# Kernel optimization log

Measured on AMD Instinct MI355X. Metric: run time of the kernel, lower is better.

The kernel has to match this reference:

```python
import jax, jax.numpy as jnp
import numpy as np

B, T, D, F = 32, 512, 512, 256
K = 3
MEL_MAX = 4096
EPS = 1e-5


def _xavier(key, shape, fan_in, fan_out):
    lim = float(np.sqrt(6.0 / (fan_in + fan_out)))
    return jax.random.uniform(key, shape, jnp.float32, -lim, lim)


def setup_inputs() -> dict:
    key = jax.random.key(0)
    ks = jax.random.split(key, 6)
    x = jax.random.normal(ks[0], (B, T, D), jnp.float32)
    target = jax.random.randint(ks[1], (B, T), 0, 8)  # per-token durations
    # conv weights stored as [K, I, O] (lax 'WIO'); torch xavier on [O,I,K]: fan_in=I*K, fan_out=O*K
    w1 = _xavier(ks[2], (K, D, F), D * K, F * K)
    b1 = jnp.zeros((F,), jnp.float32)
    g1 = jnp.ones((F,), jnp.float32)
    be1 = jnp.zeros((F,), jnp.float32)
    w2 = _xavier(ks[3], (K, F, F), F * K, F * K)
    b2 = jnp.zeros((F,), jnp.float32)
    g2 = jnp.ones((F,), jnp.float32)
    be2 = jnp.zeros((F,), jnp.float32)
    wl = _xavier(ks[4], (F, 1), F, 1)
    bl = jnp.zeros((1,), jnp.float32)
    return dict(x=x, target=target, mel_max_length=MEL_MAX,
                w1=w1, b1=b1, g1=g1, be1=be1,
                w2=w2, b2=b2, g2=g2, be2=be2, wl=wl, bl=bl)


def _layer_norm(h, g, b):
    mu = jnp.mean(h, axis=-1, keepdims=True)
    var = jnp.mean(jnp.square(h - mu), axis=-1, keepdims=True)
    return (h - mu) * jax.lax.rsqrt(var + EPS) * g + b


def _conv1d(h, w, b):
    # h: [B,T,C_in], w: [K,C_in,C_out]; torch padding=1 with K=3 == SAME
    out = jax.lax.conv_general_dilated(h, w, (1,), 'SAME',
                                       dimension_numbers=('NWC', 'WIO', 'NWC'))
    return out + b


def reference(x, target, mel_max_length, w1, b1, g1, be1, w2, b2, g2, be2, wl, bl):
    # ---- DurationPredictor (eval: dropout = identity) ----
    h = jax.nn.relu(_layer_norm(_conv1d(x, w1, b1), g1, be1))
    h = jax.nn.relu(_layer_norm(_conv1d(h, w2, b2), g2, be2))
    dur_pred = jax.nn.relu(h @ wl + bl)[..., 0]  # [B, T]

    # ---- LR: ragged expansion of x by `target` durations, padded to mel_max_length ----
    cum = jnp.cumsum(target, axis=1)              # [B, T]
    total = cum[:, -1]                            # [B]
    pos = jnp.arange(mel_max_length)              # [M]
    # frame m maps to token i with cum[i-1] <= m < cum[i]
    idx = jax.vmap(lambda c: jnp.searchsorted(c, pos, side='right'))(cum)  # [B, M]
    idx = jnp.clip(idx, 0, x.shape[1] - 1)
    mask = pos[None, :] < total[:, None]          # [B, M]
    out = jnp.take_along_axis(x, idx[..., None], axis=1) * mask[..., None].astype(x.dtype)
    return (out, dur_pred)
```

## Files before the change

### kernel.cpp

```cpp
#include <hip/hip_runtime.h>
#include <type_traits>

#define B_   32
#define T_   512
#define D_   512
#define F_   256
#define MEL  4096
#define EPS_ 1e-5f

typedef __attribute__((ext_vector_type(8))) short bf16x8;
typedef __attribute__((ext_vector_type(4))) float f32x4;

#define GLL16(gp, lp) \
    __builtin_amdgcn_global_load_lds((const __attribute__((address_space(1))) void*)(gp), \
                                     (__attribute__((address_space(3))) void*)(lp), 16, 0, 0)
#define BARRIER() do { asm volatile("" ::: "memory"); __builtin_amdgcn_s_barrier(); \
                       asm volatile("" ::: "memory"); } while (0)
#define MEMPIN() asm volatile("" ::: "memory")

__device__ inline unsigned short f2bf(float f) {
    unsigned u = __float_as_uint(f);
    unsigned r = (u + 0x7fff + ((u >> 16) & 1)) >> 16;
    return (unsigned short)r;
}

#define PREP_WBLOCKS 2304

__global__ __launch_bounds__(256)
void prep_kernel(const float* __restrict__ w1, const float* __restrict__ w2,
                 const int* __restrict__ tgt,
                 unsigned short* __restrict__ w1T, unsigned short* __restrict__ w2T,
                 int* __restrict__ gidx)
{
    __shared__ int lcum[T_];
    __shared__ int wsum[4];

    int bid = blockIdx.x;
    int tid = threadIdx.x;
    if (bid < PREP_WBLOCKS) {
        int idx = bid * 256 + tid;
        if (idx < 3 * D_ * F_) {
            int kk = idx / F_, f = idx % F_;
            w1T[(size_t)f * (3 * D_) + kk] = f2bf(w1[idx]);
        } else {
            int j = idx - 3 * D_ * F_;
            int kk = j / F_, f = j % F_;
            w2T[(size_t)f * (3 * F_) + kk] = f2bf(w2[j]);
        }
        return;
    }

    int b = bid - PREP_WBLOCKS;
    int t0 = tid * 2;
    int a0 = tgt[b * T_ + t0], a1 = tgt[b * T_ + t0 + 1];
    int lane = tid & 63, w = tid >> 6;
    int v = a0 + a1;
#pragma unroll
    for (int o = 1; o < 64; o <<= 1) { int u = __shfl_up(v, o); if (lane >= o) v += u; }
    if (lane == 63) wsum[w] = v;
    __syncthreads();
    int base = 0;
#pragma unroll
    for (int i = 0; i < 4; ++i) if (i < w) base += wsum[i];
    int incl = base + v;
    lcum[t0]     = incl - a1;
    lcum[t0 + 1] = incl;
    __syncthreads();

    int total = lcum[T_ - 1];
#pragma unroll
    for (int k = 0; k < MEL / 256; ++k) {
        int pos = tid + k * 256;
        int lo = 0, hi = T_;
        while (lo < hi) { int mid = (lo + hi) >> 1; if (lcum[mid] <= pos) lo = mid + 1; else hi = mid; }
        gidx[b * MEL + pos] = (pos < total) ? min(lo, T_ - 1) : -1;
    }
}

template<int IN_D, typename InT, bool FUSE_DUR, int GPHASES, int GBASE>
__global__ __launch_bounds__(512)
void conv_mfma_kernel(const InT* __restrict__ x, const unsigned short* __restrict__ wT,
                      const float* __restrict__ bias, const float* __restrict__ gamma,
                      const float* __restrict__ beta, unsigned short* __restrict__ out,
                      const float* __restrict__ wl, const float* __restrict__ bl,
                      float* __restrict__ dur,
                      const float* __restrict__ xf, const int* __restrict__ gidx,
                      float* __restrict__ gout)
{
    constexpr int MT = 64;
    constexpr int KT = 3 * IN_D;
    constexpr int PHASES = KT / 64;

    __shared__ __align__(16) char xs_raw[(MT + 2) * IN_D * 2];
    __shared__ __align__(16) unsigned short xsB[2 * 16384];
    __shared__ float red[MT][8];
    __shared__ float redD[MT][4];

    const int blocksPerBatch = T_ / MT;
    const int b  = blockIdx.x / blocksPerBatch;
    const int t0 = (blockIdx.x % blocksPerBatch) * MT;
    const int l  = threadIdx.x & 63;
    const int wv = threadIdx.x >> 6;
    const int fg = wv & 3;
    const int rg = wv >> 2;

    constexpr int CH = (MT + 2) * IN_D / 8;
    for (int c = threadIdx.x; c < CH; c += 512) {
        int j  = c / (IN_D / 8);
        int d8 = (c % (IN_D / 8)) * 8;
        int t  = t0 - 1 + j;
        uint4 pk = make_uint4(0u, 0u, 0u, 0u);
        if (t >= 0 && t < T_) {
            if constexpr (std::is_same_v<InT, float>) {
                const float4* src = reinterpret_cast<const float4*>(&x[((size_t)b * T_ + t) * IN_D + d8]);
                float4 a0 = src[0], a1 = src[1];
                pk.x = (unsigned)f2bf(a0.x) | ((unsigned)f2bf(a0.y) << 16);
                pk.y = (unsigned)f2bf(a0.z) | ((unsigned)f2bf(a0.w) << 16);
                pk.z = (unsigned)f2bf(a1.x) | ((unsigned)f2bf(a1.y) << 16);
                pk.w = (unsigned)f2bf(a1.z) | ((unsigned)f2bf(a1.w) << 16);
            } else {
                pk = *reinterpret_cast<const uint4*>(&x[((size_t)b * T_ + t) * IN_D + d8]);
            }
        }
        int byte = ((j * IN_D + d8) * 2) ^ ((j & 7) << 4);
        *reinterpret_cast<uint4*>(&xs_raw[byte]) = pk;
    }

    float bv[4], gv[4], bev[4], wlv[4];
#pragma unroll
    for (int n = 0; n < 4; ++n) {
        int f = fg * 64 + n * 16 + (l & 15);
        bv[n] = bias[f]; gv[n] = gamma[f]; bev[n] = beta[f];
        if constexpr (FUSE_DUR) wlv[n] = wl[f];
    }
    float blv = FUSE_DUR ? bl[0] : 0.f;

    asm volatile("s_waitcnt vmcnt(0)" ::: "memory");
    __syncthreads();

    constexpr int GROWS = 2 * GPHASES;
    const int rbase = GBASE + (blockIdx.x * 8 + wv) * GROWS;
    int gidxv = gidx[rbase + min(l, GROWS - 1)];
    MEMPIN();

    const int sbase = wv * 4;
    auto stageB = [&](int ph, int buf) {
        int p = ph < PHASES ? ph : PHASES - 1;
        unsigned short* lb = &xsB[buf * 16384];
#pragma unroll
        for (int i = 0; i < 4; ++i) {
            int s = sbase + i;
            int c = s * 64 + l;
            int f = c >> 3;
            int kg = (c & 7) ^ (f & 7);
            const unsigned short* src = wT + (size_t)f * KT + p * 64 + kg * 8;
            GLL16(src, lb + s * 512);
        }
    };
    auto loadBfrag = [&](bf16x8* dst, int buf, int kk2) {
#pragma unroll
        for (int n = 0; n < 4; ++n) {
            int f  = fg * 64 + n * 16 + (l & 15);
            int kg = kk2 * 4 + (l >> 4);
            dst[n] = *reinterpret_cast<const bf16x8*>(&xsB[buf * 16384 + f * 64 + ((kg ^ (f & 7)) * 8)]);
        }
    };
    const int k_lane = (l >> 4) * 8;
    auto loadA = [&](bf16x8* dst, int kk) {
        int kp = kk / IN_D;
        int dbase = (kk % IN_D) + k_lane;
#pragma unroll
        for (int m = 0; m < 2; ++m) {
            int j = rg * 32 + m * 16 + (l & 15) + kp;
            int byte = ((j * IN_D + dbase) * 2) ^ ((j & 7) << 4);
            dst[m] = *reinterpret_cast<const bf16x8*>(&xs_raw[byte]);
        }
    };

    float4 ga[3][2][2];
    auto loadSet = [&](int slot, int s) {
#pragma unroll
        for (int i = 0; i < 2; ++i) {
            int li = min(2 * s + i, GROWS - 1);
            int ix = __shfl(gidxv, li);
            int r  = rbase + li;
            const float* src = xf + ((size_t)(r >> 12) * T_ + max(ix, 0)) * D_ + l * 4;
            ga[slot][i][0] = *reinterpret_cast<const float4*>(src);
            ga[slot][i][1] = *reinterpret_cast<const float4*>(src + 256);
        }
    };
    auto storeSet = [&](int slot, int s) {
#pragma unroll
        for (int i = 0; i < 2; ++i) {
            int li = 2 * s + i;
            int ix = __shfl(gidxv, li);
            int r  = rbase + li;
            float4 a = ga[slot][i][0], c = ga[slot][i][1];
            if (ix < 0) { a = make_float4(0.f,0.f,0.f,0.f); c = make_float4(0.f,0.f,0.f,0.f); }
            float* d = gout + (size_t)r * D_ + l * 4;
            *reinterpret_cast<float4*>(d)       = a;
            *reinterpret_cast<float4*>(d + 256) = c;
        }
    };

    f32x4 acc[2][4];
#pragma unroll
    for (int m = 0; m < 2; ++m)
#pragma unroll
        for (int n = 0; n < 4; ++n) acc[m][n] = (f32x4){0.f, 0.f, 0.f, 0.f};

    stageB(0, 0);  MEMPIN();
    stageB(1, 1);  MEMPIN();
    loadSet(0, 0); MEMPIN();
    loadSet(1, 1); MEMPIN();
    loadSet(2, 2);

#pragma unroll
    for (int p = 0; p < PHASES; ++p) {
        if (p == 0)                asm volatile("s_waitcnt vmcnt(8)"  ::: "memory");
        else if (p == 1)           asm volatile("s_waitcnt vmcnt(16)" ::: "memory");
        else if (p < GPHASES + 1)  asm volatile("s_waitcnt vmcnt(12)" ::: "memory");
        else                       asm volatile("s_waitcnt vmcnt(4)"  ::: "memory");
        BARRIER();
        int buf = p & 1;
#pragma unroll
        for (int kk2 = 0; kk2 < 2; ++kk2) {
            int kk = p * 64 + kk2 * 32;
            bf16x8 Bv[4], Av[2];
            loadBfrag(Bv, buf, kk2);
            loadA(Av, kk);
#pragma unroll
            for (int m = 0; m < 2; ++m)
#pragma unroll
                for (int n = 0; n < 4; ++n)
                    acc[m][n] = __builtin_amdgcn_mfma_f32_16x16x32_bf16(Av[m], Bv[n], acc[m][n], 0, 0, 0);
        }
        BARRIER();
        if (p < GPHASES) {
            storeSet(p % 3, p);
            loadSet(p % 3, p + 3);
        }
        stageB(p + 2, buf);
    }

#pragma unroll
    for (int m = 0; m < 2; ++m)
#pragma unroll
        for (int q = 0; q < 4; ++q) {
            float s = 0.f, s2 = 0.f;
#pragma unroll
            for (int n = 0; n < 4; ++n) {
                float v2 = acc[m][n][q] + bv[n];
                acc[m][n][q] = v2;
                s += v2; s2 += v2 * v2;
            }
#pragma unroll
            for (int o = 1; o < 16; o <<= 1) { s += __shfl_xor(s, o); s2 += __shfl_xor(s2, o); }
            int row = rg * 32 + m * 16 + (l >> 4) * 4 + q;
            if ((l & 15) == 0) { red[row][fg * 2] = s; red[row][fg * 2 + 1] = s2; }
        }
    __syncthreads();

#pragma unroll
    for (int m = 0; m < 2; ++m)
#pragma unroll
        for (int q = 0; q < 4; ++q) {
            int row = rg * 32 + m * 16 + (l >> 4) * 4 + q;
            float s  = red[row][0] + red[row][2] + red[row][4] + red[row][6];
            float s2 = red[row][1] + red[row][3] + red[row][5] + red[row][7];
            float mu  = s * (1.f / F_);
            float var = s2 * (1.f / F_) - mu * mu;
            float rs  = rsqrtf(var + EPS_);
            size_t rb2 = ((size_t)(b * T_ + t0 + row)) * F_;
            float part = 0.f;
#pragma unroll
            for (int n = 0; n < 4; ++n) {
                float y = (acc[m][n][q] - mu) * rs * gv[n] + bev[n];
                y = fmaxf(y, 0.f);
                out[rb2 + fg * 64 + n * 16 + (l & 15)] = f2bf(y);
                if constexpr (FUSE_DUR) part = fmaf(y, wlv[n], part);
            }
            if constexpr (FUSE_DUR) {
#pragma unroll
                for (int o = 1; o < 16; o <<= 1) part += __shfl_xor(part, o);
                if ((l & 15) == 0) redD[row][fg] = part;
            }
        }

    if constexpr (FUSE_DUR) {
        __syncthreads();
        if (threadIdx.x < MT) {
            float s = redD[threadIdx.x][0] + redD[threadIdx.x][1]
                    + redD[threadIdx.x][2] + redD[threadIdx.x][3] + blv;
            dur[(size_t)b * T_ + t0 + threadIdx.x] = fmaxf(s, 0.f);
        }
    }
}

extern "C" void kernel_launch(void* const* d_in, const int* in_sizes, int n_in,
                              void* d_out, int out_size, void* d_ws, size_t ws_size,
                              hipStream_t stream)
{
    const float* x      = (const float*)d_in[0];
    const int*   target = (const int*)d_in[1];
    const float* w1  = (const float*)d_in[3];
    const float* b1  = (const float*)d_in[4];
    const float* g1  = (const float*)d_in[5];
    const float* be1 = (const float*)d_in[6];
    const float* w2  = (const float*)d_in[7];
    const float* b2  = (const float*)d_in[8];
    const float* g2  = (const float*)d_in[9];
    const float* be2 = (const float*)d_in[10];
    const float* wl  = (const float*)d_in[11];
    const float* bl  = (const float*)d_in[12];

    float* out = (float*)d_out;
    float* dur = out + (size_t)B_ * MEL * D_;

    char* ws = (char*)d_ws;
    unsigned short* w1T = (unsigned short*)ws;         ws += (size_t)F_ * (3 * D_) * 2;
    unsigned short* w2T = (unsigned short*)ws;         ws += (size_t)F_ * (3 * F_) * 2;
    unsigned short* h1  = (unsigned short*)ws;         ws += (size_t)B_ * T_ * F_ * 2;
    unsigned short* h2  = (unsigned short*)ws;         ws += (size_t)B_ * T_ * F_ * 2;
    int*            gidx = (int*)ws;

    prep_kernel<<<PREP_WBLOCKS + B_, 256, 0, stream>>>(w1, w2, target, w1T, w2T, gidx);

    conv_mfma_kernel<D_, float, false, 24, 0><<<B_ * (T_ / 64), 512, 0, stream>>>(
        x, w1T, b1, g1, be1, h1, nullptr, nullptr, nullptr, x, gidx, out);
    conv_mfma_kernel<F_, unsigned short, true, 8, 98304><<<B_ * (T_ / 64), 512, 0, stream>>>(
        h1, w2T, b2, g2, be2, h2, wl, bl, dur, x, gidx, out);
}
```

Before: 95.23 us.

## Merge prep and both conv stages into one cooperative kernel with grid syncs

Replaces the three separate launches (weight transpose and index prep, conv1, conv2) with one persistent cooperative kernel of 256 blocks that uses grid.sync between stages. This removes launch gaps and kernel-boundary drains. It also rebalances the gather-copy work between the two conv phases (22 versus 10 phases), skips loads for masked rows, and reorders the per-phase issue order with recomputed waitcnt values. The cost is grid-wide barriers, a shared-memory struct sized for the larger conv, and a requirement that all 256 blocks stay co-resident.

```diff
diff --git a/kernel.cpp b/kernel.cpp
--- a/kernel.cpp
+++ b/kernel.cpp
@@ -1,5 +1,8 @@
 #include <hip/hip_runtime.h>
+#include <hip/hip_cooperative_groups.h>
 #include <type_traits>
+
+namespace cg = cooperative_groups;
 
 #define B_   32
 #define T_   512
@@ -24,77 +27,26 @@
     return (unsigned short)r;
 }
 
-#define PREP_WBLOCKS 2304
-
-__global__ __launch_bounds__(256)
-void prep_kernel(const float* __restrict__ w1, const float* __restrict__ w2,
-                 const int* __restrict__ tgt,
-                 unsigned short* __restrict__ w1T, unsigned short* __restrict__ w2T,
-                 int* __restrict__ gidx)
-{
-    __shared__ int lcum[T_];
-    __shared__ int wsum[4];
-
-    int bid = blockIdx.x;
-    int tid = threadIdx.x;
-    if (bid < PREP_WBLOCKS) {
-        int idx = bid * 256 + tid;
-        if (idx < 3 * D_ * F_) {
-            int kk = idx / F_, f = idx % F_;
-            w1T[(size_t)f * (3 * D_) + kk] = f2bf(w1[idx]);
-        } else {
-            int j = idx - 3 * D_ * F_;
-            int kk = j / F_, f = j % F_;
-            w2T[(size_t)f * (3 * F_) + kk] = f2bf(w2[j]);
-        }
-        return;
-    }
-
-    int b = bid - PREP_WBLOCKS;
-    int t0 = tid * 2;
-    int a0 = tgt[b * T_ + t0], a1 = tgt[b * T_ + t0 + 1];
-    int lane = tid & 63, w = tid >> 6;
-    int v = a0 + a1;
-#pragma unroll
-    for (int o = 1; o < 64; o <<= 1) { int u = __shfl_up(v, o); if (lane >= o) v += u; }
-    if (lane == 63) wsum[w] = v;
-    __syncthreads();
-    int base = 0;
-#pragma unroll
-    for (int i = 0; i < 4; ++i) if (i < w) base += wsum[i];
-    int incl = base + v;
-    lcum[t0]     = incl - a1;
-    lcum[t0 + 1] = incl;
-    __syncthreads();
-
-    int total = lcum[T_ - 1];
-#pragma unroll
-    for (int k = 0; k < MEL / 256; ++k) {
-        int pos = tid + k * 256;
-        int lo = 0, hi = T_;
-        while (lo < hi) { int mid = (lo + hi) >> 1; if (lcum[mid] <= pos) lo = mid + 1; else hi = mid; }
-        gidx[b * MEL + pos] = (pos < total) ? min(lo, T_ - 1) : -1;
-    }
-}
-
-template<int IN_D, typename InT, bool FUSE_DUR, int GPHASES, int GBASE>
-__global__ __launch_bounds__(512)
-void conv_mfma_kernel(const InT* __restrict__ x, const unsigned short* __restrict__ wT,
-                      const float* __restrict__ bias, const float* __restrict__ gamma,
-                      const float* __restrict__ beta, unsigned short* __restrict__ out,
-                      const float* __restrict__ wl, const float* __restrict__ bl,
-                      float* __restrict__ dur,
-                      const float* __restrict__ xf, const int* __restrict__ gidx,
-                      float* __restrict__ gout)
+struct SharedMem {
+    alignas(16) char xs_raw[(64 + 2) * 512 * 2];
+    alignas(16) unsigned short xsB[2 * 16384];
+    float red[64][8];
+    float redD[64][4];
+};
+
+template<int IN_D, typename InT, bool FUSE_DUR, int GP, int GBASE>
+__device__ void conv_phase(SharedMem& sm, const InT* __restrict__ x,
+                           const unsigned short* __restrict__ wT,
+                           const float* __restrict__ bias, const float* __restrict__ gamma,
+                           const float* __restrict__ beta, unsigned short* __restrict__ outp,
+                           const float* __restrict__ wl, const float* __restrict__ bl,
+                           float* __restrict__ dur,
+                           const float* __restrict__ xf, const int* __restrict__ gidx,
+                           float* __restrict__ gout)
 {
     constexpr int MT = 64;
     constexpr int KT = 3 * IN_D;
     constexpr int PHASES = KT / 64;
-
-    __shared__ __align__(16) char xs_raw[(MT + 2) * IN_D * 2];
-    __shared__ __align__(16) unsigned short xsB[2 * 16384];
-    __shared__ float red[MT][8];
-    __shared__ float redD[MT][4];
 
     const int blocksPerBatch = T_ / MT;
     const int b  = blockIdx.x / blocksPerBatch;
@@ -123,7 +75,7 @@
             }
         }
         int byte = ((j * IN_D + d8) * 2) ^ ((j & 7) << 4);
-        *reinterpret_cast<uint4*>(&xs_raw[byte]) = pk;
+        *reinterpret_cast<uint4*>(&sm.xs_raw[byte]) = pk;
     }
 
     float bv[4], gv[4], bev[4], wlv[4];
@@ -133,12 +85,13 @@
         bv[n] = bias[f]; gv[n] = gamma[f]; bev[n] = beta[f];
         if constexpr (FUSE_DUR) wlv[n] = wl[f];
     }
-    float blv = FUSE_DUR ? bl[0] : 0.f;
+    float blv = 0.f;
+    if constexpr (FUSE_DUR) blv = bl[0];
 
     asm volatile("s_waitcnt vmcnt(0)" ::: "memory");
     __syncthreads();
 
-    constexpr int GROWS = 2 * GPHASES;
+    constexpr int GROWS = 2 * GP;
     const int rbase = GBASE + (blockIdx.x * 8 + wv) * GROWS;
     int gidxv = gidx[rbase + min(l, GROWS - 1)];
     MEMPIN();
@@ -146,7 +99,7 @@
     const int sbase = wv * 4;
     auto stageB = [&](int ph, int buf) {
         int p = ph < PHASES ? ph : PHASES - 1;
-        unsigned short* lb = &xsB[buf * 16384];
+        unsigned short* lb = &sm.xsB[buf * 16384];
 #pragma unroll
         for (int i = 0; i < 4; ++i) {
             int s = sbase + i;
@@ -162,7 +115,7 @@
         for (int n = 0; n < 4; ++n) {
             int f  = fg * 64 + n * 16 + (l & 15);
             int kg = kk2 * 4 + (l >> 4);
-            dst[n] = *reinterpret_cast<const bf16x8*>(&xsB[buf * 16384 + f * 64 + ((kg ^ (f & 7)) * 8)]);
+            dst[n] = *reinterpret_cast<const bf16x8*>(&sm.xsB[buf * 16384 + f * 64 + ((kg ^ (f & 7)) * 8)]);
         }
     };
     const int k_lane = (l >> 4) * 8;
@@ -173,33 +126,34 @@
         for (int m = 0; m < 2; ++m) {
             int j = rg * 32 + m * 16 + (l & 15) + kp;
             int byte = ((j * IN_D + dbase) * 2) ^ ((j & 7) << 4);
-            dst[m] = *reinterpret_cast<const bf16x8*>(&xs_raw[byte]);
+            dst[m] = *reinterpret_cast<const bf16x8*>(&sm.xs_raw[byte]);
         }
     };
 
     float4 ga[3][2][2];
     auto loadSet = [&](int slot, int s) {
-#pragma unroll
-        for (int i = 0; i < 2; ++i) {
-            int li = min(2 * s + i, GROWS - 1);
-            int ix = __shfl(gidxv, li);
-            int r  = rbase + li;
-            const float* src = xf + ((size_t)(r >> 12) * T_ + max(ix, 0)) * D_ + l * 4;
-            ga[slot][i][0] = *reinterpret_cast<const float4*>(src);
-            ga[slot][i][1] = *reinterpret_cast<const float4*>(src + 256);
-        }
-    };
-    auto storeSet = [&](int slot, int s) {
 #pragma unroll
         for (int i = 0; i < 2; ++i) {
             int li = 2 * s + i;
             int ix = __shfl(gidxv, li);
             int r  = rbase + li;
-            float4 a = ga[slot][i][0], c = ga[slot][i][1];
-            if (ix < 0) { a = make_float4(0.f,0.f,0.f,0.f); c = make_float4(0.f,0.f,0.f,0.f); }
+            if (ix >= 0) {
+                const float* src = xf + ((size_t)(r >> 12) * T_ + ix) * D_ + l * 4;
+                ga[slot][i][0] = *reinterpret_cast<const float4*>(src);
+                ga[slot][i][1] = *reinterpret_cast<const float4*>(src + 256);
+            } else {
+                ga[slot][i][0] = make_float4(0.f, 0.f, 0.f, 0.f);
+                ga[slot][i][1] = make_float4(0.f, 0.f, 0.f, 0.f);
+            }
+        }
+    };
+    auto storeSet = [&](int slot, int s) {
+#pragma unroll
+        for (int i = 0; i < 2; ++i) {
+            int r = rbase + 2 * s + i;
             float* d = gout + (size_t)r * D_ + l * 4;
-            *reinterpret_cast<float4*>(d)       = a;
-            *reinterpret_cast<float4*>(d + 256) = c;
+            *reinterpret_cast<float4*>(d)       = ga[slot][i][0];
+            *reinterpret_cast<float4*>(d + 256) = ga[slot][i][1];
         }
     };
 
@@ -213,14 +167,19 @@
     stageB(1, 1);  MEMPIN();
     loadSet(0, 0); MEMPIN();
     loadSet(1, 1); MEMPIN();
-    loadSet(2, 2);
+    loadSet(2, 2); MEMPIN();
 
 #pragma unroll
     for (int p = 0; p < PHASES; ++p) {
-        if (p == 0)                asm volatile("s_waitcnt vmcnt(8)"  ::: "memory");
-        else if (p == 1)           asm volatile("s_waitcnt vmcnt(16)" ::: "memory");
-        else if (p < GPHASES + 1)  asm volatile("s_waitcnt vmcnt(12)" ::: "memory");
-        else                       asm volatile("s_waitcnt vmcnt(4)"  ::: "memory");
+        const int nw = (p == 0) ? 16 : (p == 1) ? 24
+                     : (((p - 2 < GP) ? 4 : 0) + ((p + 1 < GP) ? 4 : 0) + 4 +
+                        ((p - 1 < GP) ? 4 : 0) + ((p + 2 < GP) ? 4 : 0));
+        if      (nw == 24) asm volatile("s_waitcnt vmcnt(24)" ::: "memory");
+        else if (nw == 20) asm volatile("s_waitcnt vmcnt(20)" ::: "memory");
+        else if (nw == 16) asm volatile("s_waitcnt vmcnt(16)" ::: "memory");
+        else if (nw == 12) asm volatile("s_waitcnt vmcnt(12)" ::: "memory");
+        else if (nw == 8)  asm volatile("s_waitcnt vmcnt(8)"  ::: "memory");
+        else               asm volatile("s_waitcnt vmcnt(4)"  ::: "memory");
         BARRIER();
         int buf = p & 1;
 #pragma unroll
@@ -236,11 +195,9 @@
                     acc[m][n] = __builtin_amdgcn_mfma_f32_16x16x32_bf16(Av[m], Bv[n], acc[m][n], 0, 0, 0);
         }
         BARRIER();
-        if (p < GPHASES) {
-            storeSet(p % 3, p);
-            loadSet(p % 3, p + 3);
-        }
-        stageB(p + 2, buf);
+        stageB(p + 2, buf);                       MEMPIN();
+        if (p < GP)     { storeSet(p % 3, p);     MEMPIN(); }
+        if (p + 3 < GP) { loadSet((p + 3) % 3, p + 3); MEMPIN(); }
     }
 
 #pragma unroll
@@ -257,7 +214,7 @@
 #pragma unroll
             for (int o = 1; o < 16; o <<= 1) { s += __shfl_xor(s, o); s2 += __shfl_xor(s2, o); }
             int row = rg * 32 + m * 16 + (l >> 4) * 4 + q;
-            if ((l & 15) == 0) { red[row][fg * 2] = s; red[row][fg * 2 + 1] = s2; }
+            if ((l & 15) == 0) { sm.red[row][fg * 2] = s; sm.red[row][fg * 2 + 1] = s2; }
         }
     __syncthreads();
 
@@ -266,8 +223,8 @@
 #pragma unroll
         for (int q = 0; q < 4; ++q) {
             int row = rg * 32 + m * 16 + (l >> 4) * 4 + q;
-            float s  = red[row][0] + red[row][2] + red[row][4] + red[row][6];
-            float s2 = red[row][1] + red[row][3] + red[row][5] + red[row][7];
+            float s  = sm.red[row][0] + sm.red[row][2] + sm.red[row][4] + sm.red[row][6];
+            float s2 = sm.red[row][1] + sm.red[row][3] + sm.red[row][5] + sm.red[row][7];
             float mu  = s * (1.f / F_);
             float var = s2 * (1.f / F_) - mu * mu;
             float rs  = rsqrtf(var + EPS_);
@@ -277,24 +234,91 @@
             for (int n = 0; n < 4; ++n) {
                 float y = (acc[m][n][q] - mu) * rs * gv[n] + bev[n];
                 y = fmaxf(y, 0.f);
-                out[rb2 + fg * 64 + n * 16 + (l & 15)] = f2bf(y);
+                outp[rb2 + fg * 64 + n * 16 + (l & 15)] = f2bf(y);
                 if constexpr (FUSE_DUR) part = fmaf(y, wlv[n], part);
             }
             if constexpr (FUSE_DUR) {
 #pragma unroll
                 for (int o = 1; o < 16; o <<= 1) part += __shfl_xor(part, o);
-                if ((l & 15) == 0) redD[row][fg] = part;
+                if ((l & 15) == 0) sm.redD[row][fg] = part;
             }
         }
 
     if constexpr (FUSE_DUR) {
         __syncthreads();
         if (threadIdx.x < MT) {
-            float s = redD[threadIdx.x][0] + redD[threadIdx.x][1]
-                    + redD[threadIdx.x][2] + redD[threadIdx.x][3] + blv;
+            float s = sm.redD[threadIdx.x][0] + sm.redD[threadIdx.x][1]
+                    + sm.redD[threadIdx.x][2] + sm.redD[threadIdx.x][3] + blv;
             dur[(size_t)b * T_ + t0 + threadIdx.x] = fmaxf(s, 0.f);
         }
     }
+}
+
+__global__ __launch_bounds__(512, 2)
+void mega_kernel(const float* __restrict__ x, const int* __restrict__ target,
+                 const float* __restrict__ w1, const float* __restrict__ b1,
+                 const float* __restrict__ g1, const float* __restrict__ be1,
+                 const float* __restrict__ w2, const float* __restrict__ b2,
+                 const float* __restrict__ g2, const float* __restrict__ be2,
+                 const float* __restrict__ wl, const float* __restrict__ bl,
+                 float* __restrict__ out, float* __restrict__ dur,
+                 unsigned short* __restrict__ w1T, unsigned short* __restrict__ w2T,
+                 unsigned short* __restrict__ h1, unsigned short* __restrict__ h2,
+                 int* __restrict__ gidx)
+{
+    __shared__ SharedMem sm;
+    cg::grid_group grid = cg::this_grid();
+
+    {
+        constexpr int NW1 = 3 * D_ * F_;
+        constexpr int NW2 = 3 * F_ * F_;
+        int gtid = blockIdx.x * 512 + threadIdx.x;
+        for (int i = gtid; i < NW1 + NW2; i += 256 * 512) {
+            if (i < NW1) {
+                int kk = i / F_, f = i % F_;
+                w1T[(size_t)f * (3 * D_) + kk] = f2bf(w1[i]);
+            } else {
+                int j = i - NW1;
+                int kk = j / F_, f = j % F_;
+                w2T[(size_t)f * (3 * F_) + kk] = f2bf(w2[j]);
+            }
+        }
+        if (blockIdx.x < B_) {
+            int* lcum = (int*)sm.xs_raw;
+            int* wpre = (int*)sm.redD;
+            int b = blockIdx.x;
+            int tid = threadIdx.x;
+            int lane = tid & 63, w = tid >> 6;
+            int v = target[b * T_ + tid];
+#pragma unroll
+            for (int o = 1; o < 64; o <<= 1) { int u = __shfl_up(v, o); if (lane >= o) v += u; }
+            if (lane == 63) wpre[w] = v;
+            __syncthreads();
+            int base = 0;
+#pragma unroll
+            for (int i = 0; i < 8; ++i) if (i < w) base += wpre[i];
+            lcum[tid] = base + v;
+            __syncthreads();
+            int total = lcum[T_ - 1];
+#pragma unroll
+            for (int k = 0; k < MEL / 512; ++k) {
+                int pos = tid + k * 512;
+                int lo = 0, hi = T_;
+                while (lo < hi) { int mid = (lo + hi) >> 1; if (lcum[mid] <= pos) lo = mid + 1; else hi = mid; }
+                gidx[b * MEL + pos] = (pos < total) ? min(lo, T_ - 1) : -1;
+            }
+        }
+    }
+    __threadfence();
+    grid.sync();
+
+    conv_phase<D_, float, false, 22, 0>(sm, x, w1T, b1, g1, be1, h1,
+                                        nullptr, nullptr, nullptr, x, gidx, out);
+    __threadfence();
+    grid.sync();
+
+    conv_phase<F_, unsigned short, true, 10, 90112>(sm, h1, w2T, b2, g2, be2, h2,
+                                                    wl, bl, dur, x, gidx, out);
 }
 
 extern "C" void kernel_launch(void* const* d_in, const int* in_sizes, int n_in,
@@ -324,10 +348,14 @@
     unsigned short* h2  = (unsigned short*)ws;         ws += (size_t)B_ * T_ * F_ * 2;
     int*            gidx = (int*)ws;
 
-    prep_kernel<<<PREP_WBLOCKS + B_, 256, 0, stream>>>(w1, w2, target, w1T, w2T, gidx);
-
-    conv_mfma_kernel<D_, float, false, 24, 0><<<B_ * (T_ / 64), 512, 0, stream>>>(
-        x, w1T, b1, g1, be1, h1, nullptr, nullptr, nullptr, x, gidx, out);
-    conv_mfma_kernel<F_, unsigned short, true, 8, 98304><<<B_ * (T_ / 64), 512, 0, stream>>>(
-        h1, w2T, b2, g2, be2, h2, wl, bl, dur, x, gidx, out);
+    void* args[] = {
+        (void*)&x, (void*)&target,
+        (void*)&w1, (void*)&b1, (void*)&g1, (void*)&be1,
+        (void*)&w2, (void*)&b2, (void*)&g2, (void*)&be2,
+        (void*)&wl, (void*)&bl,
+        (void*)&out, (void*)&dur,
+        (void*)&w1T, (void*)&w2T, (void*)&h1, (void*)&h2, (void*)&gidx
+    };
+    hipLaunchCooperativeKernel((const void*)mega_kernel, dim3(B_ * (T_ / 64)), dim3(512),
+                               args, 0, stream);
 }
```

New measurement: 282.1 us. 2.96x slower.

## Halve conv M-tile to 32 rows and rebalance fused gather split

Applied to the files above, without the earlier changes.

Cuts the conv tile from 64 to 32 time steps, which doubles the grid and halves the K step per phase. The B staging layout moves to a k-major, unswizzled form, and launch bounds now request 4 blocks per CU. The gather rows interleaved with the two conv kernels are redistributed (22 and 10 rows per wave) to match the new block count. The aim is more occupancy and parallelism, paid for with more weight reloads per block, more barriers per unit of MFMA work, and possible LDS bank conflicts from the unswizzled B layout.

```diff
diff --git a/kernel.cpp b/kernel.cpp
--- a/kernel.cpp
+++ b/kernel.cpp
@@ -77,8 +77,8 @@
     }
 }
 
-template<int IN_D, typename InT, bool FUSE_DUR, int GPHASES, int GBASE>
-__global__ __launch_bounds__(512)
+template<int IN_D, typename InT, bool FUSE_DUR, int GP, int GBASE>
+__global__ __launch_bounds__(512, 4)
 void conv_mfma_kernel(const InT* __restrict__ x, const unsigned short* __restrict__ wT,
                       const float* __restrict__ bias, const float* __restrict__ gamma,
                       const float* __restrict__ beta, unsigned short* __restrict__ out,
@@ -87,12 +87,12 @@
                       const float* __restrict__ xf, const int* __restrict__ gidx,
                       float* __restrict__ gout)
 {
-    constexpr int MT = 64;
+    constexpr int MT = 32;
     constexpr int KT = 3 * IN_D;
-    constexpr int PHASES = KT / 64;
+    constexpr int PHASES = KT / 32;
 
     __shared__ __align__(16) char xs_raw[(MT + 2) * IN_D * 2];
-    __shared__ __align__(16) unsigned short xsB[2 * 16384];
+    __shared__ __align__(16) unsigned short xsB[2 * 8192];
     __shared__ float red[MT][8];
     __shared__ float redD[MT][4];
 
@@ -133,159 +133,139 @@
         bv[n] = bias[f]; gv[n] = gamma[f]; bev[n] = beta[f];
         if constexpr (FUSE_DUR) wlv[n] = wl[f];
     }
-    float blv = FUSE_DUR ? bl[0] : 0.f;
+    float blv = 0.f;
+    if constexpr (FUSE_DUR) blv = bl[0];
 
     asm volatile("s_waitcnt vmcnt(0)" ::: "memory");
     __syncthreads();
 
-    constexpr int GROWS = 2 * GPHASES;
-    const int rbase = GBASE + (blockIdx.x * 8 + wv) * GROWS;
-    int gidxv = gidx[rbase + min(l, GROWS - 1)];
+    const int rbase = GBASE + (blockIdx.x * 8 + wv) * GP;
+    int gidxv = gidx[rbase + min(l, GP - 1)];
     MEMPIN();
 
-    const int sbase = wv * 4;
     auto stageB = [&](int ph, int buf) {
         int p = ph < PHASES ? ph : PHASES - 1;
-        unsigned short* lb = &xsB[buf * 16384];
-#pragma unroll
-        for (int i = 0; i < 4; ++i) {
-            int s = sbase + i;
-            int c = s * 64 + l;
-            int f = c >> 3;
-            int kg = (c & 7) ^ (f & 7);
-            const unsigned short* src = wT + (size_t)f * KT + p * 64 + kg * 8;
-            GLL16(src, lb + s * 512);
-        }
-    };
-    auto loadBfrag = [&](bf16x8* dst, int buf, int kk2) {
+        unsigned short* lb = &xsB[buf * 8192];
+#pragma unroll
+        for (int i = 0; i < 2; ++i) {
+            int c  = i * 512 + wv * 64 + l;
+            int f  = c & 255;
+            int kg = c >> 8;
+            const unsigned short* src = wT + (size_t)f * KT + p * 32 + kg * 8;
+            GLL16(src, lb + (size_t)(i * 512 + wv * 64) * 8);
+        }
+    };
+    auto loadBfrag = [&](bf16x8* dst, int buf) {
 #pragma unroll
         for (int n = 0; n < 4; ++n) {
             int f  = fg * 64 + n * 16 + (l & 15);
-            int kg = kk2 * 4 + (l >> 4);
-            dst[n] = *reinterpret_cast<const bf16x8*>(&xsB[buf * 16384 + f * 64 + ((kg ^ (f & 7)) * 8)]);
+            int kg = l >> 4;
+            dst[n] = *reinterpret_cast<const bf16x8*>(&xsB[buf * 8192 + (kg * 256 + f) * 8]);
         }
     };
     const int k_lane = (l >> 4) * 8;
     auto loadA = [&](bf16x8* dst, int kk) {
         int kp = kk / IN_D;
         int dbase = (kk % IN_D) + k_lane;
-#pragma unroll
-        for (int m = 0; m < 2; ++m) {
-            int j = rg * 32 + m * 16 + (l & 15) + kp;
-            int byte = ((j * IN_D + dbase) * 2) ^ ((j & 7) << 4);
-            dst[m] = *reinterpret_cast<const bf16x8*>(&xs_raw[byte]);
-        }
-    };
-
-    float4 ga[3][2][2];
+        int j = rg * 16 + (l & 15) + kp;
+        int byte = ((j * IN_D + dbase) * 2) ^ ((j & 7) << 4);
+        dst[0] = *reinterpret_cast<const bf16x8*>(&xs_raw[byte]);
+    };
+
+    float4 ga[3][2];
     auto loadSet = [&](int slot, int s) {
-#pragma unroll
-        for (int i = 0; i < 2; ++i) {
-            int li = min(2 * s + i, GROWS - 1);
-            int ix = __shfl(gidxv, li);
-            int r  = rbase + li;
-            const float* src = xf + ((size_t)(r >> 12) * T_ + max(ix, 0)) * D_ + l * 4;
-            ga[slot][i][0] = *reinterpret_cast<const float4*>(src);
-            ga[slot][i][1] = *reinterpret_cast<const float4*>(src + 256);
-        }
+        int ix = __shfl(gidxv, s);
+        int r  = rbase + s;
+        const float* src = xf + ((size_t)(r >> 12) * T_ + max(ix, 0)) * D_ + l * 4;
+        ga[slot][0] = *reinterpret_cast<const float4*>(src);
+        ga[slot][1] = *reinterpret_cast<const float4*>(src + 256);
     };
     auto storeSet = [&](int slot, int s) {
-#pragma unroll
-        for (int i = 0; i < 2; ++i) {
-            int li = 2 * s + i;
-            int ix = __shfl(gidxv, li);
-            int r  = rbase + li;
-            float4 a = ga[slot][i][0], c = ga[slot][i][1];
-            if (ix < 0) { a = make_float4(0.f,0.f,0.f,0.f); c = make_float4(0.f,0.f,0.f,0.f); }
-            float* d = gout + (size_t)r * D_ + l * 4;
-            *reinterpret_cast<float4*>(d)       = a;
-            *reinterpret_cast<float4*>(d + 256) = c;
-        }
-    };
-
-    f32x4 acc[2][4];
-#pragma unroll
-    for (int m = 0; m < 2; ++m)
-#pragma unroll
-        for (int n = 0; n < 4; ++n) acc[m][n] = (f32x4){0.f, 0.f, 0.f, 0.f};
+        int ix = __shfl(gidxv, s);
+        int r  = rbase + s;
+        float4 a = ga[slot][0], c = ga[slot][1];
+        if (ix < 0) { a = make_float4(0.f,0.f,0.f,0.f); c = make_float4(0.f,0.f,0.f,0.f); }
+        float* d = gout + (size_t)r * D_ + l * 4;
+        *reinterpret_cast<float4*>(d)       = a;
+        *reinterpret_cast<float4*>(d + 256) = c;
+    };
+
+    f32x4 acc[4];
+#pragma unroll
+    for (int n = 0; n < 4; ++n) acc[n] = (f32x4){0.f, 0.f, 0.f, 0.f};
 
     stageB(0, 0);  MEMPIN();
     stageB(1, 1);  MEMPIN();
     loadSet(0, 0); MEMPIN();
     loadSet(1, 1); MEMPIN();
-    loadSet(2, 2);
+    loadSet(2, 2); MEMPIN();
 
 #pragma unroll
     for (int p = 0; p < PHASES; ++p) {
-        if (p == 0)                asm volatile("s_waitcnt vmcnt(8)"  ::: "memory");
-        else if (p == 1)           asm volatile("s_waitcnt vmcnt(16)" ::: "memory");
-        else if (p < GPHASES + 1)  asm volatile("s_waitcnt vmcnt(12)" ::: "memory");
-        else                       asm volatile("s_waitcnt vmcnt(4)"  ::: "memory");
+        const int nw = (p == 0) ? 8 : (p == 1) ? 12
+                     : 2 * (1 + ((p - 2 < GP) ? 1 : 0) + ((p + 1 < GP) ? 1 : 0) +
+                                ((p - 1 < GP) ? 1 : 0) + ((p + 2 < GP) ? 1 : 0));
+        if      (nw == 12) asm volatile("s_waitcnt vmcnt(12)" ::: "memory");
+        else if (nw == 10) asm volatile("s_waitcnt vmcnt(10)" ::: "memory");
+        else if (nw == 8)  asm volatile("s_waitcnt vmcnt(8)"  ::: "memory");
+        else if (nw == 6)  asm volatile("s_waitcnt vmcnt(6)"  ::: "memory");
+        else if (nw == 4)  asm volatile("s_waitcnt vmcnt(4)"  ::: "memory");
+        else               asm volatile("s_waitcnt vmcnt(2)"  ::: "memory");
         BARRIER();
         int buf = p & 1;
-#pragma unroll
-        for (int kk2 = 0; kk2 < 2; ++kk2) {
-            int kk = p * 64 + kk2 * 32;
-            bf16x8 Bv[4], Av[2];
-            loadBfrag(Bv, buf, kk2);
-            loadA(Av, kk);
-#pragma unroll
-            for (int m = 0; m < 2; ++m)
-#pragma unroll
-                for (int n = 0; n < 4; ++n)
-                    acc[m][n] = __builtin_amdgcn_mfma_f32_16x16x32_bf16(Av[m], Bv[n], acc[m][n], 0, 0, 0);
+        {
+            bf16x8 Bv[4], Av[1];
+            loadBfrag(Bv, buf);
+            loadA(Av, p * 32);
+#pragma unroll
+            for (int n = 0; n < 4; ++n)
+                acc[n] = __builtin_amdgcn_mfma_f32_16x16x32_bf16(Av[0], Bv[n], acc[n], 0, 0, 0);
         }
         BARRIER();
-        if (p < GPHASES) {
-            storeSet(p % 3, p);
-            loadSet(p % 3, p + 3);
-        }
-        stageB(p + 2, buf);
-    }
-
-#pragma unroll
-    for (int m = 0; m < 2; ++m)
-#pragma unroll
-        for (int q = 0; q < 4; ++q) {
-            float s = 0.f, s2 = 0.f;
-#pragma unroll
-            for (int n = 0; n < 4; ++n) {
-                float v2 = acc[m][n][q] + bv[n];
-                acc[m][n][q] = v2;
-                s += v2; s2 += v2 * v2;
-            }
-#pragma unroll
-            for (int o = 1; o < 16; o <<= 1) { s += __shfl_xor(s, o); s2 += __shfl_xor(s2, o); }
-            int row = rg * 32 + m * 16 + (l >> 4) * 4 + q;
-            if ((l & 15) == 0) { red[row][fg * 2] = s; red[row][fg * 2 + 1] = s2; }
-        }
+        stageB(p + 2, buf);                            MEMPIN();
+        if (p < GP)     { storeSet(p % 3, p);          MEMPIN(); }
+        if (p + 3 < GP) { loadSet((p + 3) % 3, p + 3); MEMPIN(); }
+    }
+
+#pragma unroll
+    for (int q = 0; q < 4; ++q) {
+        float s = 0.f, s2 = 0.f;
+#pragma unroll
+        for (int n = 0; n < 4; ++n) {
+            float v2 = acc[n][q] + bv[n];
+            acc[n][q] = v2;
+            s += v2; s2 += v2 * v2;
+        }
+#pragma unroll
+        for (int o = 1; o < 16; o <<= 1) { s += __shfl_xor(s, o); s2 += __shfl_xor(s2, o); }
+        int row = rg * 16 + (l >> 4) * 4 + q;
+        if ((l & 15) == 0) { red[row][fg * 2] = s; red[row][fg * 2 + 1] = s2; }
+    }
     __syncthreads();
 
 #pragma unroll
-    for (int m = 0; m < 2; ++m)
-#pragma unroll
-        for (int q = 0; q < 4; ++q) {
-            int row = rg * 32 + m * 16 + (l >> 4) * 4 + q;
-            float s  = red[row][0] + red[row][2] + red[row][4] + red[row][6];
-            float s2 = red[row][1] + red[row][3] + red[row][5] + red[row][7];
-            float mu  = s * (1.f / F_);
-            float var = s2 * (1.f / F_) - mu * mu;
-            float rs  = rsqrtf(var + EPS_);
-            size_t rb2 = ((size_t)(b * T_ + t0 + row)) * F_;
-            float part = 0.f;
-#pragma unroll
-            for (int n = 0; n < 4; ++n) {
-                float y = (acc[m][n][q] - mu) * rs * gv[n] + bev[n];
-                y = fmaxf(y, 0.f);
-                out[rb2 + fg * 64 + n * 16 + (l & 15)] = f2bf(y);
-                if constexpr (FUSE_DUR) part = fmaf(y, wlv[n], part);
-            }
-            if constexpr (FUSE_DUR) {
-#pragma unroll
-                for (int o = 1; o < 16; o <<= 1) part += __shfl_xor(part, o);
-                if ((l & 15) == 0) redD[row][fg] = part;
-            }
-        }
+    for (int q = 0; q < 4; ++q) {
+        int row = rg * 16 + (l >> 4) * 4 + q;
+        float s  = red[row][0] + red[row][2] + red[row][4] + red[row][6];
+        float s2 = red[row][1] + red[row][3] + red[row][5] + red[row][7];
+        float mu  = s * (1.f / F_);
+        float var = s2 * (1.f / F_) - mu * mu;
+        float rs  = rsqrtf(var + EPS_);
+        size_t rb2 = ((size_t)(b * T_ + t0 + row)) * F_;
+        float part = 0.f;
+#pragma unroll
+        for (int n = 0; n < 4; ++n) {
+            float y = (acc[n][q] - mu) * rs * gv[n] + bev[n];
+            y = fmaxf(y, 0.f);
+            out[rb2 + fg * 64 + n * 16 + (l & 15)] = f2bf(y);
+            if constexpr (FUSE_DUR) part = fmaf(y, wlv[n], part);
+        }
+        if constexpr (FUSE_DUR) {
+#pragma unroll
+            for (int o = 1; o < 16; o <<= 1) part += __shfl_xor(part, o);
+            if ((l & 15) == 0) redD[row][fg] = part;
+        }
+    }
 
     if constexpr (FUSE_DUR) {
         __syncthreads();
@@ -326,8 +306,8 @@
 
     prep_kernel<<<PREP_WBLOCKS + B_, 256, 0, stream>>>(w1, w2, target, w1T, w2T, gidx);
 
-    conv_mfma_kernel<D_, float, false, 24, 0><<<B_ * (T_ / 64), 512, 0, stream>>>(
+    conv_mfma_kernel<D_, float, false, 22, 0><<<B_ * (T_ / 32), 512, 0, stream>>>(
         x, w1T, b1, g1, be1, h1, nullptr, nullptr, nullptr, x, gidx, out);
-    conv_mfma_kernel<F_, unsigned short, true, 8, 98304><<<B_ * (T_ / 64), 512, 0, stream>>>(
+    conv_mfma_kernel<F_, unsigned short, true, 10, 90112><<<B_ * (T_ / 32), 512, 0, stream>>>(
         h1, w2T, b2, g2, be2, h2, wl, bl, dur, x, gidx, out);
 }
```

Result: slower. 179.5 us (+88.5%).
